# Kernel tuning notes

Hardware: AMD Instinct MI355X
Metric: run time of the kernel (lower is better)

Reference implementation:

```python
import jax, jax.numpy as jnp
import numpy as np

N_NODES = 50000
N_EDGES = 600000
HID = 128
OUT = 14
LAYERS = 3
N_GRAPHS = 16
NODE_VOCAB = (120, 6)
EDGE_VOCAB = (6, 3)
GEN_EPS = 1e-7   # GENConv eps added after ReLU on messages
BN_EPS = 1e-5    # torch BatchNorm1d default eps


def setup_inputs() -> dict:
    key = jax.random.key(0)
    ks = jax.random.split(key, 14)
    inp = {}
    inp['node_feat0'] = jax.random.randint(ks[0], (N_NODES,), 0, NODE_VOCAB[0], dtype=jnp.int32)
    inp['node_feat1'] = jax.random.randint(ks[1], (N_NODES,), 0, NODE_VOCAB[1], dtype=jnp.int32)
    inp['edge_feat0'] = jax.random.randint(ks[2], (N_EDGES,), 0, EDGE_VOCAB[0], dtype=jnp.int32)
    inp['edge_feat1'] = jax.random.randint(ks[3], (N_EDGES,), 0, EDGE_VOCAB[1], dtype=jnp.int32)
    inp['edge_src'] = jax.random.randint(ks[4], (N_EDGES,), 0, N_NODES, dtype=jnp.int32)
    inp['edge_dst'] = jax.random.randint(ks[5], (N_EDGES,), 0, N_NODES, dtype=jnp.int32)
    inp['graph_ids'] = jnp.repeat(jnp.arange(N_GRAPHS, dtype=jnp.int32), N_NODES // N_GRAPHS)
    inp['num_graphs'] = N_GRAPHS
    s = 0.05
    inp['W_node0'] = jax.random.normal(ks[6], (NODE_VOCAB[0], HID), jnp.float32) * s
    inp['W_node1'] = jax.random.normal(ks[7], (NODE_VOCAB[1], HID), jnp.float32) * s
    # per-layer edge embedding tables (each GENConv layer has its own)
    inp['edge_emb0'] = jax.random.normal(ks[8], (LAYERS, EDGE_VOCAB[0], HID), jnp.float32) * s
    inp['edge_emb1'] = jax.random.normal(ks[9], (LAYERS, EDGE_VOCAB[1], HID), jnp.float32) * s
    inp['beta'] = jnp.ones((LAYERS,), jnp.float32)  # learnable softmax temperature, init 1.0
    inp['mlp_W'] = jax.random.normal(ks[10], (LAYERS, HID, HID), jnp.float32) * (1.0 / np.sqrt(HID))
    inp['mlp_b'] = jnp.zeros((LAYERS, HID), jnp.float32)
    inp['bn_gamma'] = jnp.ones((LAYERS, HID), jnp.float32)
    inp['bn_beta'] = jnp.zeros((LAYERS, HID), jnp.float32)
    inp['W_out'] = jax.random.normal(ks[11], (HID, OUT), jnp.float32) * (1.0 / np.sqrt(HID))
    inp['b_out'] = jnp.zeros((OUT,), jnp.float32)
    return inp


def _segment_softmax(z, seg, num_segments):
    # DGL edge_softmax: elementwise softmax over edges sharing a destination node.
    zmax = jax.ops.segment_max(z, seg, num_segments=num_segments)
    zmax = jnp.where(jnp.isfinite(zmax), zmax, 0.0)  # guard empty segments
    e = jnp.exp(z - zmax[seg])
    denom = jax.ops.segment_sum(e, seg, num_segments=num_segments)
    return e / denom[seg]


def reference(node_feat0, node_feat1, edge_feat0, edge_feat1, edge_src, edge_dst,
              graph_ids, num_graphs, W_node0, W_node1, edge_emb0, edge_emb1,
              beta, mlp_W, mlp_b, bn_gamma, bn_beta, W_out, b_out):
    # node embedding lookup + sum over tables
    hv = W_node0[node_feat0] + W_node1[node_feat1]          # [N, H]
    n = hv.shape[0]
    for l in range(mlp_W.shape[0]):
        # BatchNorm1d (training mode: batch stats, biased variance) + ReLU
        mu = jnp.mean(hv, axis=0)
        var = jnp.var(hv, axis=0)
        hv1 = (hv - mu) * jax.lax.rsqrt(var + BN_EPS) * bn_gamma[l] + bn_beta[l]
        hv1 = jax.nn.relu(hv1)
        # GENConv: edge embed sum, u_add_e, relu+eps, edge_softmax, scatter-sum
        ee = edge_emb0[l][edge_feat0] + edge_emb1[l][edge_feat1]   # [E, H]
        m = jax.nn.relu(hv1[edge_src] + ee) + GEN_EPS              # [E, H]
        a = _segment_softmax(m * beta[l], edge_dst, n)             # [E, H]
        agg = jax.ops.segment_sum(m * a, edge_dst, num_segments=n)  # [N, H]
        # feats = node_feats + msg, then 1-layer MLP, then outer skip connect
        hv = (hv1 + agg) @ mlp_W[l] + mlp_b[l] + hv
    # AvgPooling over each graph in the batch, then output Linear
    counts = jax.ops.segment_sum(jnp.ones((n,), hv.dtype), graph_ids, num_segments=num_graphs)
    hg = jax.ops.segment_sum(hv, graph_ids, num_segments=num_graphs) / counts[:, None]
    return hg @ W_out + b_out  # [num_graphs, OUT]
```

## Files before the change

kernel.cpp:

```cpp
#include <hip/hip_runtime.h>

#define N_NODESC 50000
#define N_EDGESC 600000
#define HID 128
#define LAYERS 3
#define N_GRAPHSC 16
#define OUT_DIM 14
#define GEN_EPS 1e-7f
#define BN_EPS 1e-5f
#define SCAN_BLK 196
#define EMB_BLK 6250
#define WF_BLK 192
#define CNT_BLK 2344
#define GEMM_BLK 782
#define BNR_BLK 64
#define LOG2E 1.44269504f

typedef short bf16x8 __attribute__((ext_vector_type(8)));
typedef float f32x4 __attribute__((ext_vector_type(4)));

__device__ __forceinline__ unsigned short f2bf(float f) {
    union { float f; unsigned u; } v; v.f = f;
    unsigned r = v.u + 0x7FFF + ((v.u >> 16) & 1);
    return (unsigned short)(r >> 16);
}
__device__ __forceinline__ float bf_lo(unsigned u) {
    return __uint_as_float(u << 16);
}
__device__ __forceinline__ float bf_hi(unsigned u) {
    return __uint_as_float(u & 0xFFFF0000u);
}
__device__ __forceinline__ float bfs(unsigned short u) {
    return __uint_as_float(((unsigned)u) << 16);
}

__global__ void k_blocksum(const int* __restrict__ deg, int* __restrict__ part) {
    __shared__ int sh[256];
    int t = threadIdx.x;
    int i = blockIdx.x * 256 + t;
    sh[t] = (i < N_NODESC) ? deg[i] : 0;
    __syncthreads();
    for (int off = 128; off > 0; off >>= 1) {
        if (t < off) sh[t] += sh[t + off];
        __syncthreads();
    }
    if (t == 0) part[blockIdx.x] = sh[0];
}

__global__ void k_scanpart(const int* __restrict__ part, int* __restrict__ bofs) {
    __shared__ int sh[256];
    int t = threadIdx.x;
    int v = (t < SCAN_BLK) ? part[t] : 0;
    sh[t] = v;
    __syncthreads();
    for (int off = 1; off < 256; off <<= 1) {
        int add = (t >= off) ? sh[t - off] : 0;
        __syncthreads();
        sh[t] += add;
        __syncthreads();
    }
    if (t < SCAN_BLK) bofs[t] = sh[t] - v;
}

__global__ void k_rowptr(const int* __restrict__ deg, const int* __restrict__ bofs,
                         int* __restrict__ row_ptr, int* __restrict__ cursor) {
    __shared__ int sh[256];
    int t = threadIdx.x;
    int i = blockIdx.x * 256 + t;
    int d = (i < N_NODESC) ? deg[i] : 0;
    sh[t] = d;
    __syncthreads();
    for (int off = 1; off < 256; off <<= 1) {
        int add = (t >= off) ? sh[t - off] : 0;
        __syncthreads();
        sh[t] += add;
        __syncthreads();
    }
    if (i < N_NODESC) {
        int rp = bofs[blockIdx.x] + sh[t] - d;
        row_ptr[i] = rp;
        cursor[i] = rp;
    }
    if (i == 0) row_ptr[N_NODESC] = N_EDGESC;
}

__global__ void k_scatter(const int* __restrict__ dst, const int* __restrict__ src,
                          const int* __restrict__ f0, const int* __restrict__ f1,
                          int* __restrict__ cursor, int* __restrict__ csr_pack) {
    int i = blockIdx.x * blockDim.x + threadIdx.x;
    if (i < N_EDGESC) {
        int pos = atomicAdd(&cursor[dst[i]], 1);
        csr_pack[pos] = (src[i] << 8) | ((f0[i] * 3 + f1[i]) * 8);
    }
}

__global__ void k_embed(const int* __restrict__ f0, const int* __restrict__ f1,
                        const float4* __restrict__ W0, const float4* __restrict__ W1,
                        uint2* __restrict__ hvb2, float* __restrict__ part,
                        const float* __restrict__ W, unsigned short* __restrict__ wf,
                        const int* __restrict__ edst, int* __restrict__ deg) {
    int tid = threadIdx.x;
    if (blockIdx.x >= EMB_BLK + WF_BLK) {
        int e = (blockIdx.x - EMB_BLK - WF_BLK) * 256 + tid;
        if (e < N_EDGESC) atomicAdd(&deg[edst[e]], 1);
        return;
    }
    if (blockIdx.x >= EMB_BLK) {
        int i = (blockIdx.x - EMB_BLK) * 256 + tid;
        if (i < LAYERS * 16384) {
            int j = i & 7;
            int lane = (i >> 3) & 63;
            int nt = (i >> 9) & 7;
            int ks = (i >> 12) & 3;
            int l = i >> 14;
            int k = ks * 32 + (lane >> 4) * 8 + j;
            int n = nt * 16 + (lane & 15);
            wf[i] = f2bf(W[(size_t)l * HID * HID + k * HID + n]);
        }
        return;
    }
    __shared__ float sh[1024], sh2[1024];
    int i = blockIdx.x * 256 + tid;
    int v = i >> 5, c4 = i & 31;
    float4 a = W0[f0[v] * 32 + c4];
    float4 b = W1[f1[v] * 32 + c4];
    float4 o = make_float4(a.x + b.x, a.y + b.y, a.z + b.z, a.w + b.w);
    uint2 ob;
    ob.x = (unsigned)f2bf(o.x) | ((unsigned)f2bf(o.y) << 16);
    ob.y = (unsigned)f2bf(o.z) | ((unsigned)f2bf(o.w) << 16);
    hvb2[i] = ob;
    sh[tid * 4 + 0] = o.x; sh2[tid * 4 + 0] = o.x * o.x;
    sh[tid * 4 + 1] = o.y; sh2[tid * 4 + 1] = o.y * o.y;
    sh[tid * 4 + 2] = o.z; sh2[tid * 4 + 2] = o.z * o.z;
    sh[tid * 4 + 3] = o.w; sh2[tid * 4 + 3] = o.w * o.w;
    __syncthreads();
    if (tid < 128) {
        int c4i = tid >> 2, j = tid & 3;
        float s = 0.f, s2 = 0.f;
#pragma unroll
        for (int r = 0; r < 8; r++) {
            s += sh[(r * 32 + c4i) * 4 + j];
            s2 += sh2[(r * 32 + c4i) * 4 + j];
        }
        part[(size_t)blockIdx.x * 256 + tid] = s;
        part[(size_t)blockIdx.x * 256 + 128 + tid] = s2;
    }
}

__global__ void k_bn_reduce2(const float* __restrict__ part, int nparts,
                             float* __restrict__ gsum) {
    int t = threadIdx.x;
    int rows = (nparts + BNR_BLK - 1) / BNR_BLK;
    int r0 = blockIdx.x * rows;
    int r1 = min(r0 + rows, nparts);
    float s = 0.f;
    for (int p = r0; p < r1; p++) s += part[(size_t)p * 256 + t];
    atomicAdd(&gsum[t], s);
}

__global__ __launch_bounds__(512) void k_aggemm(
    const unsigned* __restrict__ hin, unsigned short* __restrict__ hout,
    const int* __restrict__ row_ptr, const int* __restrict__ csr_pack,
    const float* __restrict__ e0, const float* __restrict__ e1,
    const float* __restrict__ beta_p, const unsigned short* __restrict__ wf,
    const float* __restrict__ b, const float* __restrict__ gsum,
    const float* __restrict__ gamma, const float* __restrict__ betab,
    float* __restrict__ gsum_next, float* __restrict__ hg) {
    __shared__ float2 sh_et[18 * 64];
    __shared__ unsigned x_tile[64 * 64];
    __shared__ float shs[512], shs2[512];
    int tid = threadIdx.x;
    for (int i = tid; i < 18 * 64; i += 512) {
        int f = i >> 6, ln = i & 63;
        int a = f / 3, bb = f - 3 * a;
        float2 ea = *(const float2*)(e0 + a * HID + 2 * ln);
        float2 eb = *(const float2*)(e1 + bb * HID + 2 * ln);
        sh_et[i] = make_float2(ea.x + eb.x, ea.y + eb.y);
    }
    int w = tid >> 6, lane = tid & 63;
    int m0 = blockIdx.x * 64;
    const float bl2 = (*beta_p) * LOG2E;
    const float invN = 1.f / (float)N_NODESC;
    int cch = lane * 2;
    float mu0 = gsum[cch] * invN, mu1 = gsum[cch + 1] * invN;
    float var0 = gsum[128 + cch] * invN - mu0 * mu0;
    float var1 = gsum[129 + cch] * invN - mu1 * mu1;
    float sc0 = gamma[cch] * rsqrtf(var0 + BN_EPS);
    float sc1 = gamma[cch + 1] * rsqrtf(var1 + BN_EPS);
    float sf0 = betab[cch] - mu0 * sc0;
    float sf1 = betab[cch + 1] - mu1 * sc1;
    __syncthreads();

    const char* hinc = (const char*)hin;
    const char* etc = (const char*)sh_et;
    unsigned lane4 = (unsigned)lane * 4;
    unsigned lane8 = (unsigned)lane * 8;

#define AGG_BODY(J)                                                         \
    {                                                                       \
        int pack = __shfl(pk, (J), 64);                                     \
        unsigned u = *(const unsigned*)(hinc +                              \
                        ((((unsigned)pack) & 0xFFFFFF00u) + lane4));        \
        float2 t = *(const float2*)(etc +                                   \
                        (((((unsigned)pack) & 0xFFu) << 6) + lane8));       \
        float a0 = fmaxf(fmaf(bf_lo(u), sc0, sf0), 0.f);                    \
        float a1 = fmaxf(fmaf(bf_hi(u), sc1, sf1), 0.f);                    \
        float r0 = fmaxf(a0 + t.x, 0.f);                                    \
        float r1 = fmaxf(a1 + t.y, 0.f);                                    \
        float w0 = exp2f(r0 * bl2);                                         \
        float w1 = exp2f(r1 * bl2);                                         \
        d0 += w0; d1 += w1;                                                 \
        n0 = fmaf(r0, w0, n0); n1 = fmaf(r1, w1, n1);                       \
    }

    for (int i = 0; i < 8; i++) {
        int row = w * 8 + i;
        int v = m0 + row;
        int vc = min(v, N_NODESC - 1);
        unsigned su = hin[(size_t)vc * 64 + lane];
        float h10 = fmaxf(fmaf(bf_lo(su), sc0, sf0), 0.f);
        float h11 = fmaxf(fmaf(bf_hi(su), sc1, sf1), 0.f);
        int p0 = row_ptr[vc];
        int deg = (v < N_NODESC) ? (row_ptr[vc + 1] - p0) : 0;
        float n0 = 0.f, n1 = 0.f, d0 = 0.f, d1 = 0.f;
        for (int base = 0; base < deg; base += 64) {
            int idx = base + lane;
            int pk = (idx < deg) ? csr_pack[p0 + idx] : 0;
            int jn = min(64, deg - base);
            int j = 0;
            for (; j + 2 <= jn; j += 2) {
                AGG_BODY(j)
                AGG_BODY(j + 1)
            }
            if (j < jn) AGG_BODY(j)
        }
        float ox = h10 + (deg ? __fdividef(n0, d0) + GEN_EPS : 0.f);
        float oy = h11 + (deg ? __fdividef(n1, d1) + GEN_EPS : 0.f);
        x_tile[row * 64 + ((lane + row * 4) & 63)] =
            (unsigned)f2bf(ox) | ((unsigned)f2bf(oy) << 16);
    }
#undef AGG_BODY
    __syncthreads();

    int rw = w & 3, chh = w >> 2;
    int mrow = lane & 15, grp = lane >> 4;
    int rbase = rw * 16 + mrow;
    bf16x8 af[4];
#pragma unroll
    for (int ks = 0; ks < 4; ks++) {
        int col = ks * 16 + grp * 4;
        int colr = (col + rbase * 4) & 63;
        af[ks] = *(const bf16x8*)&x_tile[rbase * 64 + colr];
    }
    f32x4 acc[4];
#pragma unroll
    for (int nt = 0; nt < 4; nt++) acc[nt] = (f32x4){0.f, 0.f, 0.f, 0.f};
#pragma unroll
    for (int nt = 0; nt < 4; nt++) {
        int ntg = chh * 4 + nt;
#pragma unroll
        for (int ks = 0; ks < 4; ks++) {
            bf16x8 bfr = *(const bf16x8*)(wf +
                (size_t)((ks * 8 + ntg) * 64 + lane) * 8);
            acc[nt] = __builtin_amdgcn_mfma_f32_16x16x32_bf16(
                af[ks], bfr, acc[nt], 0, 0, 0);
        }
    }
    const unsigned short* hin_s = (const unsigned short*)hin;
    int gA = m0 / 3125;
    int boundary = (gA + 1) * 3125;
#pragma unroll
    for (int nt = 0; nt < 4; nt++) {
        int col = chh * 64 + nt * 16 + mrow;
        float bias = b[col];
        float s = 0.f, s2 = 0.f;
#pragma unroll
        for (int r = 0; r < 4; r++) {
            int v = m0 + rw * 16 + grp * 4 + r;
            if (v < N_NODESC) {
                size_t idx = (size_t)v * HID + col;
                float o = acc[nt][r] + bias + bfs(hin_s[idx]);
                hout[idx] = f2bf(o);
                if (hg) {
                    if (v < boundary) s += o; else s2 += o;
                } else {
                    s += o; s2 += o * o;
                }
            }
        }
        s  += __shfl_xor(s, 16, 64);  s  += __shfl_xor(s, 32, 64);
        s2 += __shfl_xor(s2, 16, 64); s2 += __shfl_xor(s2, 32, 64);
        if (lane < 16) { shs[rw * 128 + col] = s; shs2[rw * 128 + col] = s2; }
    }
    __syncthreads();
    if (hg) {
        int gB = min(m0 + 63, N_NODESC - 1) / 3125;
        if (tid < 128) {
            atomicAdd(&hg[gA * 128 + tid],
                shs[tid] + shs[128 + tid] + shs[256 + tid] + shs[384 + tid]);
        } else if (tid < 256 && gB != gA) {
            int c = tid - 128;
            atomicAdd(&hg[gB * 128 + c],
                shs2[c] + shs2[128 + c] + shs2[256 + c] + shs2[384 + c]);
        }
    } else if (gsum_next) {
        if (tid < 128) {
            atomicAdd(&gsum_next[tid],
                shs[tid] + shs[128 + tid] + shs[256 + tid] + shs[384 + tid]);
        } else if (tid < 256) {
            int c = tid - 128;
            atomicAdd(&gsum_next[tid],
                shs2[c] + shs2[128 + c] + shs2[256 + c] + shs2[384 + c]);
        }
    }
}

__global__ void k_finish(const float* __restrict__ hg, const float* __restrict__ Wo,
                         const float* __restrict__ bo, float* __restrict__ out) {
    int t = threadIdx.x;
    if (t >= N_GRAPHSC * OUT_DIM) return;
    int g = t / OUT_DIM, o = t % OUT_DIM;
    const float inv = (float)N_GRAPHSC / (float)N_NODESC;
    float acc = bo[o];
    for (int k = 0; k < HID; k++)
        acc += hg[g * HID + k] * inv * Wo[k * OUT_DIM + o];
    out[t] = acc;
}

extern "C" void kernel_launch(void* const* d_in, const int* in_sizes, int n_in,
                              void* d_out, int out_size, void* d_ws, size_t ws_size,
                              hipStream_t stream) {
    const int* node_feat0 = (const int*)d_in[0];
    const int* node_feat1 = (const int*)d_in[1];
    const int* edge_feat0 = (const int*)d_in[2];
    const int* edge_feat1 = (const int*)d_in[3];
    const int* edge_src   = (const int*)d_in[4];
    const int* edge_dst   = (const int*)d_in[5];
    const float* W_node0   = (const float*)d_in[8];
    const float* W_node1   = (const float*)d_in[9];
    const float* edge_emb0 = (const float*)d_in[10];
    const float* edge_emb1 = (const float*)d_in[11];
    const float* beta      = (const float*)d_in[12];
    const float* mlp_W     = (const float*)d_in[13];
    const float* mlp_b     = (const float*)d_in[14];
    const float* bn_gamma  = (const float*)d_in[15];
    const float* bn_beta   = (const float*)d_in[16];
    const float* W_out     = (const float*)d_in[17];
    const float* b_out     = (const float*)d_in[18];
    float* out = (float*)d_out;

    char* ws = (char*)d_ws;
    size_t off = 0;
    auto alloc = [&](size_t bytes) -> void* {
        void* p = ws + off;
        off += (bytes + 255) & ~(size_t)255;
        return p;
    };
    unsigned short* hvA = (unsigned short*)alloc((size_t)N_NODESC * HID * 2);
    unsigned short* hvB = (unsigned short*)alloc((size_t)N_NODESC * HID * 2);
    float* gsums   = (float*)alloc(LAYERS * 256 * 4);
    float* hg      = (float*)alloc(N_GRAPHSC * HID * 4);
    float* bnpart  = (float*)alloc((size_t)EMB_BLK * 256 * 4);
    unsigned short* wfrag = (unsigned short*)alloc((size_t)LAYERS * 16384 * 2);
    int* row_ptr   = (int*)alloc((N_NODESC + 1) * 4);
    int* cursor    = (int*)alloc(N_NODESC * 4);
    int* deg       = (int*)alloc(N_NODESC * 4);
    int* part      = (int*)alloc(SCAN_BLK * 4);
    int* bofs      = (int*)alloc(SCAN_BLK * 4);
    int* csr_pack  = (int*)alloc((size_t)N_EDGESC * 4);

    hipMemsetAsync(deg, 0, N_NODESC * 4, stream);
    hipMemsetAsync(gsums, 0, LAYERS * 256 * 4 + N_GRAPHSC * HID * 4, stream);

    k_embed<<<EMB_BLK + WF_BLK + CNT_BLK, 256, 0, stream>>>(
        node_feat0, node_feat1, (const float4*)W_node0, (const float4*)W_node1,
        (uint2*)hvA, bnpart, mlp_W, wfrag, edge_dst, deg);

    k_blocksum<<<SCAN_BLK, 256, 0, stream>>>(deg, part);
    k_scanpart<<<1, 256, 0, stream>>>(part, bofs);
    k_rowptr<<<SCAN_BLK, 256, 0, stream>>>(deg, bofs, row_ptr, cursor);
    k_scatter<<<(N_EDGESC + 255) / 256, 256, 0, stream>>>(
        edge_dst, edge_src, edge_feat0, edge_feat1, cursor, csr_pack);

    k_bn_reduce2<<<BNR_BLK, 256, 0, stream>>>(bnpart, EMB_BLK, gsums);

    unsigned short* hin = hvA;
    unsigned short* hout = hvB;
    for (int l = 0; l < LAYERS; l++) {
        float* gsum = gsums + l * 256;
        float* gnext = (l + 1 < LAYERS) ? gsums + (l + 1) * 256 : nullptr;
        float* hgp = (l == LAYERS - 1) ? hg : nullptr;
        k_aggemm<<<GEMM_BLK, 512, 0, stream>>>(
            (const unsigned*)hin, hout, row_ptr, csr_pack,
            edge_emb0 + (size_t)l * 6 * HID, edge_emb1 + (size_t)l * 3 * HID,
            beta + l, wfrag + (size_t)l * 16384, mlp_b + l * HID,
            gsum, bn_gamma + l * HID, bn_beta + l * HID, gnext, hgp);
        unsigned short* tmp = hin; hin = hout; hout = tmp;
    }

    k_finish<<<1, 256, 0, stream>>>(hg, W_out, b_out, out);
}
```

Before: 416.0 us.

## Split wavefront into half-waves processing two edges at once with 4 channels per lane

The aggregation loop now has each half of the 64-lane wavefront handle a different incoming edge. Each lane covers 4 channels through 8-byte bf16 loads and 16-byte edge-table loads, and the two partial softmax sums are combined with a cross-half shuffle. The aim is to halve the serial edge iterations per node and widen the memory accesses, which should raise gather throughput. In exchange it needs more registers, uses readlane-based broadcast, and adds an odd-edge tail path plus a final reduction.

After: 435.5 us. +4.7%, slower.

```diff
diff --git a/kernel.cpp b/kernel.cpp
--- a/kernel.cpp
+++ b/kernel.cpp
@@ -166,80 +166,150 @@
     const float* __restrict__ b, const float* __restrict__ gsum,
     const float* __restrict__ gamma, const float* __restrict__ betab,
     float* __restrict__ gsum_next, float* __restrict__ hg) {
-    __shared__ float2 sh_et[18 * 64];
+    __shared__ float4 sh_et[18 * 32];
     __shared__ unsigned x_tile[64 * 64];
     __shared__ float shs[512], shs2[512];
     int tid = threadIdx.x;
-    for (int i = tid; i < 18 * 64; i += 512) {
-        int f = i >> 6, ln = i & 63;
+    for (int i = tid; i < 18 * 32; i += 512) {
+        int f = i >> 5, q = i & 31;
         int a = f / 3, bb = f - 3 * a;
-        float2 ea = *(const float2*)(e0 + a * HID + 2 * ln);
-        float2 eb = *(const float2*)(e1 + bb * HID + 2 * ln);
-        sh_et[i] = make_float2(ea.x + eb.x, ea.y + eb.y);
+        float4 ea = *(const float4*)(e0 + a * HID + 4 * q);
+        float4 eb = *(const float4*)(e1 + bb * HID + 4 * q);
+        sh_et[i] = make_float4(ea.x + eb.x, ea.y + eb.y,
+                               ea.z + eb.z, ea.w + eb.w);
     }
     int w = tid >> 6, lane = tid & 63;
+    int hw = lane >> 5, lq = lane & 31;
     int m0 = blockIdx.x * 64;
     const float bl2 = (*beta_p) * LOG2E;
     const float invN = 1.f / (float)N_NODESC;
-    int cch = lane * 2;
-    float mu0 = gsum[cch] * invN, mu1 = gsum[cch + 1] * invN;
-    float var0 = gsum[128 + cch] * invN - mu0 * mu0;
-    float var1 = gsum[129 + cch] * invN - mu1 * mu1;
-    float sc0 = gamma[cch] * rsqrtf(var0 + BN_EPS);
-    float sc1 = gamma[cch + 1] * rsqrtf(var1 + BN_EPS);
-    float sf0 = betab[cch] - mu0 * sc0;
-    float sf1 = betab[cch + 1] - mu1 * sc1;
+    int c0 = lq * 4;
+    float sc0, sc1, sc2, sc3, sf0, sf1, sf2, sf3;
+    {
+        float mu0 = gsum[c0] * invN,     mu1 = gsum[c0 + 1] * invN;
+        float mu2 = gsum[c0 + 2] * invN, mu3 = gsum[c0 + 3] * invN;
+        float v0 = gsum[128 + c0] * invN - mu0 * mu0;
+        float v1 = gsum[129 + c0] * invN - mu1 * mu1;
+        float v2 = gsum[130 + c0] * invN - mu2 * mu2;
+        float v3 = gsum[131 + c0] * invN - mu3 * mu3;
+        sc0 = gamma[c0] * rsqrtf(v0 + BN_EPS);
+        sc1 = gamma[c0 + 1] * rsqrtf(v1 + BN_EPS);
+        sc2 = gamma[c0 + 2] * rsqrtf(v2 + BN_EPS);
+        sc3 = gamma[c0 + 3] * rsqrtf(v3 + BN_EPS);
+        sf0 = betab[c0] - mu0 * sc0;
+        sf1 = betab[c0 + 1] - mu1 * sc1;
+        sf2 = betab[c0 + 2] - mu2 * sc2;
+        sf3 = betab[c0 + 3] - mu3 * sc3;
+    }
     __syncthreads();
 
     const char* hinc = (const char*)hin;
     const char* etc = (const char*)sh_et;
-    unsigned lane4 = (unsigned)lane * 4;
-    unsigned lane8 = (unsigned)lane * 8;
-
-#define AGG_BODY(J)                                                         \
+    unsigned lane8q = (unsigned)lq * 8;
+    unsigned lane16q = (unsigned)lq * 16;
+
+#define LOADS(S, JA)                                                        \
     {                                                                       \
-        int pack = __shfl(pk, (J), 64);                                     \
-        unsigned u = *(const unsigned*)(hinc +                              \
-                        ((((unsigned)pack) & 0xFFFFFF00u) + lane4));        \
-        float2 t = *(const float2*)(etc +                                   \
-                        (((((unsigned)pack) & 0xFFu) << 6) + lane8));       \
-        float a0 = fmaxf(fmaf(bf_lo(u), sc0, sf0), 0.f);                    \
-        float a1 = fmaxf(fmaf(bf_hi(u), sc1, sf1), 0.f);                    \
-        float r0 = fmaxf(a0 + t.x, 0.f);                                    \
-        float r1 = fmaxf(a1 + t.y, 0.f);                                    \
+        int pa = __builtin_amdgcn_readlane(pk, 2 * (JA));                   \
+        int pb = __builtin_amdgcn_readlane(pk, 2 * (JA) + 1);               \
+        unsigned ps = (unsigned)(hw ? pb : pa);                             \
+        uu##S = *(const uint2*)(hinc + (ps & 0xFFFFFF00u) + lane8q);        \
+        tt##S = *(const float4*)(etc + ((ps & 0xFFu) << 6) + lane16q);      \
+    }
+#define COMPS(S)                                                            \
+    {                                                                       \
+        float r0 = fmaxf(fmaxf(fmaf(bf_lo(uu##S.x), sc0, sf0), 0.f)         \
+                         + tt##S.x, 0.f);                                   \
+        float r1 = fmaxf(fmaxf(fmaf(bf_hi(uu##S.x), sc1, sf1), 0.f)         \
+                         + tt##S.y, 0.f);                                   \
+        float r2 = fmaxf(fmaxf(fmaf(bf_lo(uu##S.y), sc2, sf2), 0.f)         \
+                         + tt##S.z, 0.f);                                   \
+        float r3 = fmaxf(fmaxf(fmaf(bf_hi(uu##S.y), sc3, sf3), 0.f)         \
+                         + tt##S.w, 0.f);                                   \
         float w0 = exp2f(r0 * bl2);                                         \
         float w1 = exp2f(r1 * bl2);                                         \
-        d0 += w0; d1 += w1;                                                 \
+        float w2 = exp2f(r2 * bl2);                                         \
+        float w3 = exp2f(r3 * bl2);                                         \
+        d0 += w0; d1 += w1; d2 += w2; d3 += w3;                             \
         n0 = fmaf(r0, w0, n0); n1 = fmaf(r1, w1, n1);                       \
+        n2 = fmaf(r2, w2, n2); n3 = fmaf(r3, w3, n3);                       \
     }
 
     for (int i = 0; i < 8; i++) {
         int row = w * 8 + i;
         int v = m0 + row;
         int vc = min(v, N_NODESC - 1);
-        unsigned su = hin[(size_t)vc * 64 + lane];
-        float h10 = fmaxf(fmaf(bf_lo(su), sc0, sf0), 0.f);
-        float h11 = fmaxf(fmaf(bf_hi(su), sc1, sf1), 0.f);
+        uint2 su = *(const uint2*)(hinc + (size_t)vc * 256 + lane8q);
+        float h0 = fmaxf(fmaf(bf_lo(su.x), sc0, sf0), 0.f);
+        float h1 = fmaxf(fmaf(bf_hi(su.x), sc1, sf1), 0.f);
+        float h2 = fmaxf(fmaf(bf_lo(su.y), sc2, sf2), 0.f);
+        float h3 = fmaxf(fmaf(bf_hi(su.y), sc3, sf3), 0.f);
         int p0 = row_ptr[vc];
         int deg = (v < N_NODESC) ? (row_ptr[vc + 1] - p0) : 0;
-        float n0 = 0.f, n1 = 0.f, d0 = 0.f, d1 = 0.f;
+        float n0 = 0.f, n1 = 0.f, n2 = 0.f, n3 = 0.f;
+        float d0 = 0.f, d1 = 0.f, d2 = 0.f, d3 = 0.f;
         for (int base = 0; base < deg; base += 64) {
             int idx = base + lane;
             int pk = (idx < deg) ? csr_pack[p0 + idx] : 0;
             int jn = min(64, deg - base);
+            int full = jn >> 1;
+            uint2 uu0, uu1;
+            float4 tt0, tt1;
             int j = 0;
-            for (; j + 2 <= jn; j += 2) {
-                AGG_BODY(j)
-                AGG_BODY(j + 1)
+            for (; j + 2 <= full; j += 2) {
+                LOADS(0, j)
+                LOADS(1, j + 1)
+                COMPS(0)
+                COMPS(1)
             }
-            if (j < jn) AGG_BODY(j)
-        }
-        float ox = h10 + (deg ? __fdividef(n0, d0) + GEN_EPS : 0.f);
-        float oy = h11 + (deg ? __fdividef(n1, d1) + GEN_EPS : 0.f);
-        x_tile[row * 64 + ((lane + row * 4) & 63)] =
-            (unsigned)f2bf(ox) | ((unsigned)f2bf(oy) << 16);
-    }
-#undef AGG_BODY
+            if (j < full) {
+                LOADS(0, j)
+                COMPS(0)
+            }
+            if (jn & 1) {
+                int pe = __shfl(pk, jn - 1, 64);
+                unsigned ps = (unsigned)pe;
+                if (lane < 32) {
+                    uint2 ue = *(const uint2*)(hinc +
+                                   (ps & 0xFFFFFF00u) + lane8q);
+                    float4 te = *(const float4*)(etc +
+                                   ((ps & 0xFFu) << 6) + lane16q);
+                    float r0 = fmaxf(fmaxf(fmaf(bf_lo(ue.x), sc0, sf0), 0.f)
+                                     + te.x, 0.f);
+                    float r1 = fmaxf(fmaxf(fmaf(bf_hi(ue.x), sc1, sf1), 0.f)
+                                     + te.y, 0.f);
+                    float r2 = fmaxf(fmaxf(fmaf(bf_lo(ue.y), sc2, sf2), 0.f)
+                                     + te.z, 0.f);
+                    float r3 = fmaxf(fmaxf(fmaf(bf_hi(ue.y), sc3, sf3), 0.f)
+                                     + te.w, 0.f);
+                    float w0 = exp2f(r0 * bl2);
+                    float w1 = exp2f(r1 * bl2);
+                    float w2 = exp2f(r2 * bl2);
+                    float w3 = exp2f(r3 * bl2);
+                    d0 += w0; d1 += w1; d2 += w2; d3 += w3;
+                    n0 = fmaf(r0, w0, n0); n1 = fmaf(r1, w1, n1);
+                    n2 = fmaf(r2, w2, n2); n3 = fmaf(r3, w3, n3);
+                }
+            }
+        }
+        d0 += __shfl_xor(d0, 32, 64); n0 += __shfl_xor(n0, 32, 64);
+        d1 += __shfl_xor(d1, 32, 64); n1 += __shfl_xor(n1, 32, 64);
+        d2 += __shfl_xor(d2, 32, 64); n2 += __shfl_xor(n2, 32, 64);
+        d3 += __shfl_xor(d3, 32, 64); n3 += __shfl_xor(n3, 32, 64);
+        float ox0 = h0 + (deg ? __fdividef(n0, d0) + GEN_EPS : 0.f);
+        float ox1 = h1 + (deg ? __fdividef(n1, d1) + GEN_EPS : 0.f);
+        float ox2 = h2 + (deg ? __fdividef(n2, d2) + GEN_EPS : 0.f);
+        float ox3 = h3 + (deg ? __fdividef(n3, d3) + GEN_EPS : 0.f);
+        if (lane < 32) {
+            int colp = (lq * 2 + row * 4) & 63;
+            x_tile[row * 64 + colp] =
+                (unsigned)f2bf(ox0) | ((unsigned)f2bf(ox1) << 16);
+            x_tile[row * 64 + colp + 1] =
+                (unsigned)f2bf(ox2) | ((unsigned)f2bf(ox3) << 16);
+        }
+    }
+#undef LOADS
+#undef COMPS
     __syncthreads();
 
     int rw = w & 3, chh = w >> 2;
```
